# Kernel optimization log

Hardware: AMD Instinct MI355X
Metric: run time of the kernel (lower is better)

Reference implementation:

```python
import jax, jax.numpy as jnp
import numpy as np
import math

SEQ = 2048
D_MODEL = 1024
HEADS = 16
D_K = D_MODEL // HEADS
B = 2


def setup_inputs() -> dict:
    key = jax.random.key(0)
    k1, k2, k3, k4, k5 = jax.random.split(key, 5)
    s = 1.0 / math.sqrt(D_MODEL)
    x = jax.random.normal(k1, (B, SEQ, D_MODEL), dtype=jnp.float32)
    w_qkv = jax.random.normal(k2, (D_MODEL, 3 * D_MODEL), dtype=jnp.float32) * s
    b_qkv = jax.random.normal(k3, (3 * D_MODEL,), dtype=jnp.float32) * 0.01
    w_out = jax.random.normal(k4, (D_MODEL, D_MODEL), dtype=jnp.float32) * s
    b_out = jax.random.normal(k5, (D_MODEL,), dtype=jnp.float32) * 0.01
    return {"x": x, "w_qkv": w_qkv, "b_qkv": b_qkv, "w_out": w_out, "b_out": b_out}


def _rope_tables():
    inv_freq = 1.0 / (10000.0 ** (jnp.arange(0, D_K, 2, dtype=jnp.float32) / D_K))
    angles = jnp.arange(SEQ, dtype=jnp.float32)[:, None] * inv_freq[None, :]  # [S, d_k/2]
    return jnp.sin(angles), jnp.cos(angles)


def _apply_rope(x, sin, cos):
    # x: [H, B, S, d_k]; interleaved pairing: x1 = even lanes, x2 = odd lanes
    xp = x.reshape(*x.shape[:-1], D_K // 2, 2)
    x1, x2 = xp[..., 0], xp[..., 1]
    r1 = x1 * cos - x2 * sin
    r2 = x1 * sin + x2 * cos
    return jnp.stack([r1, r2], axis=-1).reshape(x.shape)


def reference(x, w_qkv, b_qkv, w_out, b_out):
    qkv = x @ w_qkv + b_qkv                     # [B, S, 3D]
    q, k, v = jnp.split(qkv, 3, axis=-1)        # each [B, S, D]

    def to_heads(t):  # chunk last dim into heads -> [H, B, S, d_k]
        return t.reshape(B, SEQ, HEADS, D_K).transpose(2, 0, 1, 3)

    q, k, v = to_heads(q), to_heads(k), to_heads(v)
    sin, cos = _rope_tables()
    q = _apply_rope(q, sin, cos)
    k = _apply_rope(k, sin, cos)

    # NOTE: original divides by scale = 1/sqrt(d_k) -> multiply by sqrt(d_k)
    scores = jnp.einsum('hbqd,hbkd->hbqk', q, k) * math.sqrt(D_K)
    causal = jnp.tril(jnp.ones((SEQ, SEQ), dtype=bool))
    scores = jnp.where(causal, scores, -jnp.inf)
    attn = jax.nn.softmax(scores, axis=-1)      # dropout_prob = 0.0
    out = jnp.einsum('hbqk,hbkd->hbqd', attn, v)  # [H, B, S, d_k]
    concat = out.transpose(1, 2, 0, 3).reshape(B, SEQ, D_MODEL)
    return concat @ w_out + b_out
```

## Files before the change

### kernel.cpp

```cpp
#include <hip/hip_runtime.h>


typedef __attribute__((ext_vector_type(8))) short s16x8;
typedef __attribute__((ext_vector_type(8))) unsigned short u16x8;
typedef __attribute__((ext_vector_type(4))) float f32x4;
typedef __attribute__((ext_vector_type(4))) int i32x4;

#define L2E 1.44269504088896340736f

__device__ __forceinline__ unsigned short f2bf(float f) {
  unsigned int u = __builtin_bit_cast(unsigned int, f);
  u += 0x7FFFu + ((u >> 16) & 1u);
  return (unsigned short)(u >> 16);
}
__device__ __forceinline__ float bf2f(unsigned short h) {
  unsigned int u = ((unsigned int)h) << 16;
  return __builtin_bit_cast(float, u);
}

__device__ __forceinline__ void gload16(const void* g, void* l) {
  __builtin_amdgcn_global_load_lds(
      (const __attribute__((address_space(1))) unsigned int*)g,
      (__attribute__((address_space(3))) unsigned int*)l, 16, 0, 0);
}

__global__ __launch_bounds__(256) void split_x_kernel(
    const float* __restrict__ x, unsigned short* __restrict__ xhi,
    unsigned short* __restrict__ xlo) {
  size_t i = ((size_t)blockIdx.x * 256 + threadIdx.x) * 8;
  f32x4 a = *(const f32x4*)(x + i);
  f32x4 c = *(const f32x4*)(x + i + 4);
  u16x8 h, lo;
#pragma unroll
  for (int j = 0; j < 4; ++j) {
    unsigned short hv = f2bf(a[j]);
    h[j] = hv; lo[j] = f2bf(a[j] - bf2f(hv));
    unsigned short hv2 = f2bf(c[j]);
    h[4 + j] = hv2; lo[4 + j] = f2bf(c[j] - bf2f(hv2));
  }
  *(u16x8*)(xhi + i) = h;
  *(u16x8*)(xlo + i) = lo;
}

__global__ __launch_bounds__(256) void transpose_split_kernel(
    const float* __restrict__ W, unsigned short* __restrict__ Thi,
    unsigned short* __restrict__ Tlo, int N, int hasLo) {
  __shared__ unsigned short hi[64][72];
  __shared__ unsigned short lo[64][72];
  const int t = threadIdx.x;
  const int k0 = blockIdx.x * 64, n0 = blockIdx.y * 64;
#pragma unroll
  for (int r = 0; r < 16; ++r) {
    int kk = r * 4 + (t >> 6);
    int nn = t & 63;
    float v = W[(size_t)(k0 + kk) * N + n0 + nn];
    unsigned short hv = f2bf(v);
    hi[nn][kk] = hv;
    lo[nn][kk] = f2bf(v - bf2f(hv));
  }
  __syncthreads();
#pragma unroll
  for (int i = 0; i < 2; ++i) {
    int ci = t + i * 256;
    int nn = ci >> 3, kc = (ci & 7) * 8;
    u16x8 vh, vl;
#pragma unroll
    for (int j = 0; j < 8; ++j) { vh[j] = hi[nn][kc + j]; vl[j] = lo[nn][kc + j]; }
    *(u16x8*)(Thi + (size_t)(n0 + nn) * 1024 + k0 + kc) = vh;
    if (hasLo) *(u16x8*)(Tlo + (size_t)(n0 + nn) * 1024 + k0 + kc) = vl;
  }
}

__global__ __launch_bounds__(256) void rope_tab_kernel(float* __restrict__ tab) {
  int idx = blockIdx.x * 256 + threadIdx.x;
  int s = idx >> 5, i = idx & 31;
  float invf = exp2f(-(float)i * 0.4152410118609203f);
  float ang = (float)s * invf;
  tab[idx] = cosf(ang);
  tab[65536 + idx] = sinf(ang);
}

__global__ __launch_bounds__(256) void gemm_qkv_kernel(
    const unsigned short* __restrict__ xhi, const unsigned short* __restrict__ xlo,
    const unsigned short* __restrict__ whi, const unsigned short* __restrict__ wlo,
    const float* __restrict__ bqkv, const float* __restrict__ ctab,
    unsigned short* __restrict__ Qsb, unsigned short* __restrict__ Ksb,
    unsigned short* __restrict__ vbufT) {
  __shared__ alignas(16) unsigned short sh[32768];
  const int tid = threadIdx.x, w = tid >> 6, l = tid & 63;
  const int l15 = l & 15, l4 = l >> 4;
  const int m0 = blockIdx.x * 128, n0 = blockIdx.y * 128;
  const int wrow = w >> 1, wcol = w & 1;
  const int which = n0 >> 10;
  const bool isV = (which == 2);
  const float* stab = ctab + 65536;
  const int g_row = l >> 2;
  const int g_col = (l & 3) * 8;

  f32x4 acc[4][4] = {};

#define STAGEP(p_) do {                                                        \
    int kk_ = (p_) * 32;                                                       \
    unsigned short* lb0_ = sh + (((p_) & 1) << 14) + (w * 2) * 512;            \
    _Pragma("unroll")                                                          \
    for (int i = 0; i < 2; ++i) {                                              \
      int rb_ = (w * 2 + i) * 16 + g_row;                                      \
      unsigned short* lb_ = lb0_ + i * 512;                                    \
      gload16(xhi + (size_t)(m0 + rb_) * 1024 + kk_ + g_col, lb_);             \
      gload16(whi + (size_t)(n0 + rb_) * 1024 + kk_ + g_col, lb_ + 4096);      \
      if (!isV) {                                                              \
        gload16(wlo + (size_t)(n0 + rb_) * 1024 + kk_ + g_col, lb_ + 8192);    \
        gload16(xlo + (size_t)(m0 + rb_) * 1024 + kk_ + g_col, lb_ + 12288);   \
      }                                                                        \
    }                                                                          \
  } while (0)

  STAGEP(0);
  __syncthreads();
  for (int p = 0; p < 32; ++p) {
    if (p + 1 < 32) STAGEP(p + 1);
    const unsigned short* bp = sh + ((p & 1) << 14);
    s16x8 af[4], bfr[4];
#pragma unroll
    for (int g = 0; g < 4; ++g) {
      af[g] = *(const s16x8*)(bp + (wrow * 64 + g * 16 + l15) * 32 + l4 * 8);
      bfr[g] = *(const s16x8*)(bp + 4096 + (wcol * 64 + g * 16 + l15) * 32 + l4 * 8);
    }
#pragma unroll
    for (int rg = 0; rg < 4; ++rg)
#pragma unroll
      for (int cg = 0; cg < 4; ++cg)
        acc[rg][cg] = __builtin_amdgcn_mfma_f32_16x16x32_bf16(af[rg], bfr[cg], acc[rg][cg], 0, 0, 0);
    if (!isV) {
      s16x8 bl[4], al[4];
#pragma unroll
      for (int g = 0; g < 4; ++g) {
        bl[g] = *(const s16x8*)(bp + 8192 + (wcol * 64 + g * 16 + l15) * 32 + l4 * 8);
        al[g] = *(const s16x8*)(bp + 12288 + (wrow * 64 + g * 16 + l15) * 32 + l4 * 8);
      }
#pragma unroll
      for (int rg = 0; rg < 4; ++rg)
#pragma unroll
        for (int cg = 0; cg < 4; ++cg)
          acc[rg][cg] = __builtin_amdgcn_mfma_f32_16x16x32_bf16(af[rg], bl[cg], acc[rg][cg], 0, 0, 0);
#pragma unroll
      for (int rg = 0; rg < 4; ++rg)
#pragma unroll
        for (int cg = 0; cg < 4; ++cg)
          acc[rg][cg] = __builtin_amdgcn_mfma_f32_16x16x32_bf16(al[rg], bfr[cg], acc[rg][cg], 0, 0, 0);
    }
    __syncthreads();
  }
#undef STAGEP

  const int n_head0 = (n0 & 1023) >> 6;
  const int bb = m0 >> 11;
  const int s_base = m0 & 2047;
  unsigned short* stg = sh;

  if (isV) {
#pragma unroll
    for (int cg = 0; cg < 4; ++cg) {
      int n_local = wcol * 64 + cg * 16 + l15;
      float bias = bqkv[n0 + n_local];
      int swz = (n_local & 7) << 3;
#pragma unroll
      for (int rg = 0; rg < 4; ++rg)
#pragma unroll
        for (int r = 0; r < 4; ++r) {
          int m_local = wrow * 64 + rg * 16 + l4 * 4 + r;
          stg[n_local * 128 + (m_local ^ swz)] = f2bf(acc[rg][cg][r] + bias);
        }
    }
    __syncthreads();
#pragma unroll
    for (int i = 0; i < 8; ++i) {
      int c = i * 256 + tid;
      int n = c >> 4, piece = c & 15;
      int hh = n_head0 + (n >> 6), d = n & 63;
      unsigned short* dst =
          vbufT + ((size_t)(bb * 16 + hh)) * 131072 + d * 2048 + s_base + piece * 8;
      *(i32x4*)dst = *(const i32x4*)(stg + n * 128 + ((piece * 8) ^ ((n & 7) << 3)));
    }
  } else {
    unsigned short* qk = which ? Ksb : Qsb;
    const float sc8 = which ? 1.0f : 8.0f;
#pragma unroll
    for (int cg = 0; cg < 4; ++cg) {
      int n_local = wcol * 64 + cg * 16 + l15;
      int dk = n_local & 63;
      int ih = dk >> 1;
      float bias = bqkv[n0 + n_local];
#pragma unroll
      for (int rg = 0; rg < 4; ++rg)
#pragma unroll
        for (int r = 0; r < 4; ++r) {
          int s = s_base + wrow * 64 + rg * 16 + l4 * 4 + r;
          float v = acc[rg][cg][r] + bias;
          float p = __shfl_xor(v, 1);
          float cs = ctab[(s << 5) + ih];
          float sn = stab[(s << 5) + ih];
          float rr = (dk & 1) ? (p * sn + v * cs) : (v * cs - p * sn);
          acc[rg][cg][r] = rr * sc8;
        }
    }
#pragma unroll
    for (int pass = 0; pass < 2; ++pass) {
#pragma unroll
      for (int cg = 0; cg < 4; ++cg) {
        int n_local = wcol * 64 + cg * 16 + l15;
#pragma unroll
        for (int rg = 0; rg < 4; ++rg)
#pragma unroll
          for (int r = 0; r < 4; ++r) {
            int m_local = wrow * 64 + rg * 16 + l4 * 4 + r;
            float rr = acc[rg][cg][r];
            unsigned short hv = f2bf(rr);
            stg[m_local * 128 + n_local] = pass ? f2bf(rr - bf2f(hv)) : hv;
          }
      }
      __syncthreads();
#pragma unroll
      for (int i = 0; i < 8; ++i) {
        int c = i * 256 + tid;
        int hh_l = c >> 10, row = (c >> 3) & 127, piece = c & 7;
        int hh = n_head0 + hh_l;
        unsigned short* dst =
            qk + (((size_t)bb * 16 + hh) * 2048 + s_base + row) * 128 + pass * 64;
        *(i32x4*)(dst + piece * 8) = *(const i32x4*)(stg + row * 128 + hh_l * 64 + piece * 8);
      }
      __syncthreads();
    }
  }
}

__global__ __launch_bounds__(512, 4) void flash_kernel(
    const unsigned short* __restrict__ Qs, const unsigned short* __restrict__ Ks,
    const unsigned short* __restrict__ VbT, unsigned short* __restrict__ attn) {
  __shared__ alignas(16) unsigned short Khi[2][64 * 64];
  __shared__ alignas(16) unsigned short Klo[2][64 * 64];
  __shared__ alignas(16) unsigned short Vt[2][64 * 64];
  __shared__ alignas(16) unsigned short Pl[8][16 * 64];

  const int tid = threadIdx.x;
  const int wv = tid >> 6, l = tid & 63;
  const int l15 = l & 15, l4 = l >> 4;

  const int sid = blockIdx.x;
  const int idx = (sid & 255) >> 5;
  const int strip = (sid >> 8) ? idx : 15 - idx;
  const int hb = sid & 31;
  const int h = hb & 15, b = hb >> 4;
  const int qb = strip * 128;

  const size_t bh = (size_t)(b * 16 + h);
  const unsigned short* Qbase = Qs + bh * 2048 * 128;
  const unsigned short* Kbase = Ks + bh * 2048 * 128;
  const unsigned short* Vbase = VbT + bh * 131072;

  s16x8 qf[2][2];
  {
    int q = qb + wv * 16 + l15;
    const unsigned short* qr = Qbase + (size_t)q * 128;
#pragma unroll
    for (int ks = 0; ks < 2; ++ks) {
      qf[0][ks] = *(const s16x8*)(qr + ks * 32 + l4 * 8);
      qf[1][ks] = *(const s16x8*)(qr + 64 + ks * 32 + l4 * 8);
    }
  }

  s16x8 vones;
#pragma unroll
  for (int j = 0; j < 8; ++j) vones[j] = (short)0x3F80;

  f32x4 acc[4] = {};
  f32x4 accl = {};
  float mrow[4];
#pragma unroll
  for (int r = 0; r < 4; ++r) mrow[r] = -1e38f;

  const int row = tid >> 3;
  const int cb = (tid & 7) * 16;

  i32x4 kh, kl, vv;
#define PREF(kt_) do {                                                        \
    int kv0_ = (kt_) * 64;                                                    \
    const char* s_ = (const char*)(Kbase + (size_t)(kv0_ + row) * 128);       \
    kh = *(const i32x4*)(s_ + cb);  kl = *(const i32x4*)(s_ + 128 + cb);      \
    vv = *(const i32x4*)((const char*)(Vbase + (size_t)row * 2048 + kv0_) + cb); \
  } while (0)

#define STAGE(bf_) do {                                                       \
    int sw = cb ^ ((row & 7) << 4);                                           \
    *(i32x4*)((char*)Khi[bf_] + row * 128 + sw) = kh;                         \
    *(i32x4*)((char*)Klo[bf_] + row * 128 + sw) = kl;                         \
    *(i32x4*)((char*)Vt[bf_] + row * 128 + sw) = vv;                          \
  } while (0)

  const int nt = (qb >> 6) + 2;
  PREF(0);
  STAGE(0);
  if (nt > 1) PREF(1);
  __syncthreads();

  for (int kt = 0; kt < nt; ++kt) {
    const int kv0 = kt * 64;
    const int cur = kt & 1;
    if (kt + 1 < nt) {
      STAGE(cur ^ 1);
      if (kt + 2 < nt) PREF(kt + 2);
    }

    f32x4 sc[4];
#pragma unroll
    for (int cg = 0; cg < 4; ++cg) {
      int kr = cg * 16 + l15;
      int swz = (kr & 7) << 4;
      const char* ph = (const char*)Khi[cur] + kr * 128;
      const char* pl2 = (const char*)Klo[cur] + kr * 128;
      s16x8 kbh[2], kbl[2];
#pragma unroll
      for (int ks = 0; ks < 2; ++ks) {
        int off = (ks * 64 + l4 * 16) ^ swz;
        kbh[ks] = *(const s16x8*)(ph + off);
        kbl[ks] = *(const s16x8*)(pl2 + off);
      }
      __builtin_amdgcn_s_setprio(1);
      f32x4 a = {0.f, 0.f, 0.f, 0.f};
#pragma unroll
      for (int ks = 0; ks < 2; ++ks) {
        a = __builtin_amdgcn_mfma_f32_16x16x32_bf16(qf[0][ks], kbh[ks], a, 0, 0, 0);
        a = __builtin_amdgcn_mfma_f32_16x16x32_bf16(qf[0][ks], kbl[ks], a, 0, 0, 0);
        a = __builtin_amdgcn_mfma_f32_16x16x32_bf16(qf[1][ks], kbh[ks], a, 0, 0, 0);
      }
      __builtin_amdgcn_s_setprio(0);
      sc[cg] = a;
    }

    if (kt >= (qb >> 6)) {
#pragma unroll
      for (int cg = 0; cg < 4; ++cg)
#pragma unroll
        for (int r = 0; r < 4; ++r) {
          int q = qb + wv * 16 + l4 * 4 + r;
          int kv = kv0 + cg * 16 + l15;
          if (kv > q) sc[cg][r] = -1e38f;
        }
    }

    {
      float vmax[4];
      bool cnd = true;
#pragma unroll
      for (int r = 0; r < 4; ++r) {
        float v = fmaxf(fmaxf(sc[0][r], sc[1][r]), fmaxf(sc[2][r], sc[3][r]));
        v = fmaxf(v, __shfl_xor(v, 1));
        v = fmaxf(v, __shfl_xor(v, 2));
        v = fmaxf(v, __shfl_xor(v, 4));
        v = fmaxf(v, __shfl_xor(v, 8));
        vmax[r] = v;
        cnd = cnd && (v <= mrow[r] + 8.0f);
      }
      const bool defer = __all(cnd ? 1 : 0);
      if (!defer) {
#pragma unroll
        for (int r = 0; r < 4; ++r) {
          float mn = fmaxf(mrow[r], vmax[r]);
          float al = exp2f((mrow[r] - mn) * L2E);
          mrow[r] = mn;
          accl[r] *= al;
#pragma unroll
          for (int dg = 0; dg < 4; ++dg) acc[dg][r] *= al;
        }
      }
#pragma unroll
      for (int cg = 0; cg < 4; ++cg)
#pragma unroll
        for (int r = 0; r < 4; ++r)
          sc[cg][r] = exp2f((sc[cg][r] - mrow[r]) * L2E);
#pragma unroll
      for (int cg = 0; cg < 4; ++cg)
#pragma unroll
        for (int r = 0; r < 4; ++r) {
          int roww = l4 * 4 + r;
          int colb = (cg * 16 + l15) * 2;
          int addr = roww * 128 + (colb ^ ((roww & 7) << 4));
          *(unsigned short*)((char*)Pl[wv] + addr) = f2bf(sc[cg][r]);
        }
    }

    {
      s16x8 pf[2];
      int swz = (l15 & 7) << 4;
#pragma unroll
      for (int kc = 0; kc < 2; ++kc)
        pf[kc] = *(const s16x8*)((const char*)Pl[wv] + l15 * 128 + ((kc * 64 + l4 * 16) ^ swz));
      __builtin_amdgcn_s_setprio(1);
#pragma unroll
      for (int dg = 0; dg < 4; ++dg) {
        int dr = dg * 16 + l15;
        int swzd = (dr & 7) << 4;
#pragma unroll
        for (int kc = 0; kc < 2; ++kc) {
          s16x8 vf = *(const s16x8*)((const char*)Vt[cur] + dr * 128 + ((kc * 64 + l4 * 16) ^ swzd));
          acc[dg] = __builtin_amdgcn_mfma_f32_16x16x32_bf16(pf[kc], vf, acc[dg], 0, 0, 0);
        }
      }
#pragma unroll
      for (int kc = 0; kc < 2; ++kc)
        accl = __builtin_amdgcn_mfma_f32_16x16x32_bf16(pf[kc], vones, accl, 0, 0, 0);
      __builtin_amdgcn_s_setprio(0);
    }
    __syncthreads();
  }
#undef PREF
#undef STAGE

  {
    unsigned short* stg = (unsigned short*)Pl;
#pragma unroll
    for (int r = 0; r < 4; ++r) {
      float inv = 1.0f / accl[r];
      int row_local = wv * 16 + l4 * 4 + r;
#pragma unroll
      for (int dg = 0; dg < 4; ++dg)
        stg[row_local * 64 + dg * 16 + l15] = f2bf(acc[dg][r] * inv);
    }
    __syncthreads();
#pragma unroll
    for (int i = 0; i < 2; ++i) {
      int c = i * 512 + tid;
      int rw = c >> 3, piece = c & 7;
      unsigned short* dst = attn + ((size_t)(b * 2048 + qb + rw)) * 1024 + h * 64;
      *(i32x4*)(dst + piece * 8) = *(const i32x4*)(stg + rw * 64 + piece * 8);
    }
  }
}

__global__ __launch_bounds__(256) void gemm_out_kernel(
    const unsigned short* __restrict__ attn, const unsigned short* __restrict__ wot,
    const float* __restrict__ bout, float* __restrict__ out) {
  __shared__ alignas(16) unsigned short sh[16384];
  const int tid = threadIdx.x, w = tid >> 6, l = tid & 63;
  const int l15 = l & 15, l4 = l >> 4;
  const int m0 = blockIdx.x * 128, n0 = blockIdx.y * 128;
  const int wrow = w >> 1, wcol = w & 1;
  const int g_row = l >> 2, g_col = (l & 3) * 8;

  f32x4 acc[4][4] = {};

#define STAGEP(p_) do {                                                        \
    int kk_ = (p_) * 32;                                                       \
    unsigned short* lb0_ = sh + (((p_) & 1) << 13) + (w * 2) * 512;            \
    _Pragma("unroll")                                                          \
    for (int i = 0; i < 2; ++i) {                                              \
      int rb_ = (w * 2 + i) * 16 + g_row;                                      \
      unsigned short* lb_ = lb0_ + i * 512;                                    \
      gload16(attn + (size_t)(m0 + rb_) * 1024 + kk_ + g_col, lb_);            \
      gload16(wot + (size_t)(n0 + rb_) * 1024 + kk_ + g_col, lb_ + 4096);      \
    }                                                                          \
  } while (0)

  STAGEP(0);
  __syncthreads();
  for (int p = 0; p < 32; ++p) {
    if (p + 1 < 32) STAGEP(p + 1);
    const unsigned short* bp = sh + ((p & 1) << 13);
    s16x8 af[4], bfr[4];
#pragma unroll
    for (int g = 0; g < 4; ++g) {
      af[g] = *(const s16x8*)(bp + (wrow * 64 + g * 16 + l15) * 32 + l4 * 8);
      bfr[g] = *(const s16x8*)(bp + 4096 + (wcol * 64 + g * 16 + l15) * 32 + l4 * 8);
    }
#pragma unroll
    for (int rg = 0; rg < 4; ++rg)
#pragma unroll
      for (int cg = 0; cg < 4; ++cg)
        acc[rg][cg] = __builtin_amdgcn_mfma_f32_16x16x32_bf16(af[rg], bfr[cg], acc[rg][cg], 0, 0, 0);
    __syncthreads();
  }
#undef STAGEP

#pragma unroll
  for (int cg = 0; cg < 4; ++cg) {
    int n = n0 + wcol * 64 + cg * 16 + l15;
    float bias = bout[n];
#pragma unroll
    for (int rg = 0; rg < 4; ++rg) {
#pragma unroll
      for (int r = 0; r < 4; ++r) {
        int m = m0 + wrow * 64 + rg * 16 + l4 * 4 + r;
        out[(size_t)m * 1024 + n] = acc[rg][cg][r] + bias;
      }
    }
  }
}

#define OFF_XHI 0ull
#define OFF_ATT 0ull
#define OFF_XLO 8388608ull
#define OFF_WHI 16777216ull
#define OFF_WLO 23068672ull
#define OFF_WOT 29360128ull
#define OFF_QS  31457280ull
#define OFF_KS  48234496ull
#define OFF_V   65011712ull

extern "C" void kernel_launch(void* const* d_in, const int* in_sizes, int n_in,
                              void* d_out, int out_size, void* d_ws, size_t ws_size,
                              hipStream_t stream) {
  (void)in_sizes; (void)n_in; (void)out_size; (void)ws_size;
  const float* x     = (const float*)d_in[0];
  const float* w_qkv = (const float*)d_in[1];
  const float* b_qkv = (const float*)d_in[2];
  const float* w_out = (const float*)d_in[3];
  const float* b_out = (const float*)d_in[4];
  float* out = (float*)d_out;
  char* ws = (char*)d_ws;

  unsigned short* xhi = (unsigned short*)(ws + OFF_XHI);
  unsigned short* xlo = (unsigned short*)(ws + OFF_XLO);
  unsigned short* whi = (unsigned short*)(ws + OFF_WHI);
  unsigned short* wlo = (unsigned short*)(ws + OFF_WLO);
  unsigned short* wot = (unsigned short*)(ws + OFF_WOT);
  unsigned short* Qsb = (unsigned short*)(ws + OFF_QS);
  unsigned short* Ksb = (unsigned short*)(ws + OFF_KS);
  unsigned short* vbT = (unsigned short*)(ws + OFF_V);
  unsigned short* att = (unsigned short*)(ws + OFF_ATT);

  float* rtab = out;

  split_x_kernel<<<2048, 256, 0, stream>>>(x, xhi, xlo);
  transpose_split_kernel<<<dim3(16, 48), 256, 0, stream>>>(w_qkv, whi, wlo, 3072, 1);
  transpose_split_kernel<<<dim3(16, 16), 256, 0, stream>>>(w_out, wot, nullptr, 1024, 0);
  rope_tab_kernel<<<256, 256, 0, stream>>>(rtab);
  gemm_qkv_kernel<<<dim3(32, 24), 256, 0, stream>>>(xhi, xlo, whi, wlo, b_qkv, rtab, Qsb, Ksb, vbT);
  flash_kernel<<<512, 512, 0, stream>>>(Qsb, Ksb, vbT, att);
  gemm_out_kernel<<<dim3(32, 8), 256, 0, stream>>>(att, wot, b_out, out);
}
```

Baseline: 192.7 us.

## Load GEMM MFMA fragments directly from global memory into registers, bypassing LDS

Both the QKV and output projection GEMMs drop the LDS double-buffered staging via global_load_lds and instead load MFMA operand fragments straight from global memory into registers. A two-deep register ping-pong overlaps the next fragment loads with the current MFMAs and removes the per-iteration __syncthreads. This gives up LDS sharing, so each wave reloads A and B tiles that other waves also read, which raises global/L2 traffic and register pressure. Each lane also makes 16-byte reads strided across rows, which may coalesce worse.

```diff
diff --git a/kernel.cpp b/kernel.cpp
--- a/kernel.cpp
+++ b/kernel.cpp
@@ -16,12 +16,6 @@
 __device__ __forceinline__ float bf2f(unsigned short h) {
   unsigned int u = ((unsigned int)h) << 16;
   return __builtin_bit_cast(float, u);
-}
-
-__device__ __forceinline__ void gload16(const void* g, void* l) {
-  __builtin_amdgcn_global_load_lds(
-      (const __attribute__((address_space(1))) unsigned int*)g,
-      (__attribute__((address_space(3))) unsigned int*)l, 16, 0, 0);
 }
 
 __global__ __launch_bounds__(256) void split_x_kernel(
@@ -86,7 +80,7 @@
     const float* __restrict__ bqkv, const float* __restrict__ ctab,
     unsigned short* __restrict__ Qsb, unsigned short* __restrict__ Ksb,
     unsigned short* __restrict__ vbufT) {
-  __shared__ alignas(16) unsigned short sh[32768];
+  __shared__ alignas(16) unsigned short sh[16384];
   const int tid = threadIdx.x, w = tid >> 6, l = tid & 63;
   const int l15 = l & 15, l4 = l >> 4;
   const int m0 = blockIdx.x * 128, n0 = blockIdx.y * 128;
@@ -94,64 +88,66 @@
   const int which = n0 >> 10;
   const bool isV = (which == 2);
   const float* stab = ctab + 65536;
-  const int g_row = l >> 2;
-  const int g_col = (l & 3) * 8;
+
+  const unsigned short* Ah = xhi + (size_t)(m0 + wrow * 64 + l15) * 1024 + l4 * 8;
+  const unsigned short* Al = xlo + (size_t)(m0 + wrow * 64 + l15) * 1024 + l4 * 8;
+  const unsigned short* Bh = whi + (size_t)(n0 + wcol * 64 + l15) * 1024 + l4 * 8;
+  const unsigned short* Bl = wlo + (size_t)(n0 + wcol * 64 + l15) * 1024 + l4 * 8;
 
   f32x4 acc[4][4] = {};
 
-#define STAGEP(p_) do {                                                        \
-    int kk_ = (p_) * 32;                                                       \
-    unsigned short* lb0_ = sh + (((p_) & 1) << 14) + (w * 2) * 512;            \
+#define LOADF(ah_, bh_, al_, bl_, p_) do {                                     \
     _Pragma("unroll")                                                          \
-    for (int i = 0; i < 2; ++i) {                                              \
-      int rb_ = (w * 2 + i) * 16 + g_row;                                      \
-      unsigned short* lb_ = lb0_ + i * 512;                                    \
-      gload16(xhi + (size_t)(m0 + rb_) * 1024 + kk_ + g_col, lb_);             \
-      gload16(whi + (size_t)(n0 + rb_) * 1024 + kk_ + g_col, lb_ + 4096);      \
-      if (!isV) {                                                              \
-        gload16(wlo + (size_t)(n0 + rb_) * 1024 + kk_ + g_col, lb_ + 8192);    \
-        gload16(xlo + (size_t)(m0 + rb_) * 1024 + kk_ + g_col, lb_ + 12288);   \
+    for (int g = 0; g < 4; ++g) {                                              \
+      ah_[g] = *(const s16x8*)(Ah + g * 16384 + (p_) * 32);                    \
+      bh_[g] = *(const s16x8*)(Bh + g * 16384 + (p_) * 32);                    \
+    }                                                                          \
+    if (!isV) {                                                                \
+      _Pragma("unroll")                                                        \
+      for (int g = 0; g < 4; ++g) {                                            \
+        al_[g] = *(const s16x8*)(Al + g * 16384 + (p_) * 32);                  \
+        bl_[g] = *(const s16x8*)(Bl + g * 16384 + (p_) * 32);                  \
       }                                                                        \
     }                                                                          \
   } while (0)
 
-  STAGEP(0);
-  __syncthreads();
-  for (int p = 0; p < 32; ++p) {
-    if (p + 1 < 32) STAGEP(p + 1);
-    const unsigned short* bp = sh + ((p & 1) << 14);
-    s16x8 af[4], bfr[4];
-#pragma unroll
-    for (int g = 0; g < 4; ++g) {
-      af[g] = *(const s16x8*)(bp + (wrow * 64 + g * 16 + l15) * 32 + l4 * 8);
-      bfr[g] = *(const s16x8*)(bp + 4096 + (wcol * 64 + g * 16 + l15) * 32 + l4 * 8);
-    }
-#pragma unroll
-    for (int rg = 0; rg < 4; ++rg)
-#pragma unroll
-      for (int cg = 0; cg < 4; ++cg)
-        acc[rg][cg] = __builtin_amdgcn_mfma_f32_16x16x32_bf16(af[rg], bfr[cg], acc[rg][cg], 0, 0, 0);
-    if (!isV) {
-      s16x8 bl[4], al[4];
-#pragma unroll
-      for (int g = 0; g < 4; ++g) {
-        bl[g] = *(const s16x8*)(bp + 8192 + (wcol * 64 + g * 16 + l15) * 32 + l4 * 8);
-        al[g] = *(const s16x8*)(bp + 12288 + (wrow * 64 + g * 16 + l15) * 32 + l4 * 8);
-      }
-#pragma unroll
-      for (int rg = 0; rg < 4; ++rg)
-#pragma unroll
-        for (int cg = 0; cg < 4; ++cg)
-          acc[rg][cg] = __builtin_amdgcn_mfma_f32_16x16x32_bf16(af[rg], bl[cg], acc[rg][cg], 0, 0, 0);
-#pragma unroll
-      for (int rg = 0; rg < 4; ++rg)
-#pragma unroll
-        for (int cg = 0; cg < 4; ++cg)
-          acc[rg][cg] = __builtin_amdgcn_mfma_f32_16x16x32_bf16(al[rg], bfr[cg], acc[rg][cg], 0, 0, 0);
-    }
-    __syncthreads();
-  }
-#undef STAGEP
+#define MFMAS(ah_, bh_, al_, bl_) do {                                         \
+    _Pragma("unroll")                                                          \
+    for (int rg = 0; rg < 4; ++rg)                                             \
+      _Pragma("unroll")                                                        \
+      for (int cg = 0; cg < 4; ++cg)                                           \
+        acc[rg][cg] = __builtin_amdgcn_mfma_f32_16x16x32_bf16(                 \
+            ah_[rg], bh_[cg], acc[rg][cg], 0, 0, 0);                           \
+    if (!isV) {                                                                \
+      _Pragma("unroll")                                                        \
+      for (int rg = 0; rg < 4; ++rg)                                           \
+        _Pragma("unroll")                                                      \
+        for (int cg = 0; cg < 4; ++cg)                                         \
+          acc[rg][cg] = __builtin_amdgcn_mfma_f32_16x16x32_bf16(               \
+              ah_[rg], bl_[cg], acc[rg][cg], 0, 0, 0);                         \
+      _Pragma("unroll")                                                        \
+      for (int rg = 0; rg < 4; ++rg)                                           \
+        _Pragma("unroll")                                                      \
+        for (int cg = 0; cg < 4; ++cg)                                         \
+          acc[rg][cg] = __builtin_amdgcn_mfma_f32_16x16x32_bf16(               \
+              al_[rg], bh_[cg], acc[rg][cg], 0, 0, 0);                         \
+    }                                                                          \
+  } while (0)
+
+  {
+    s16x8 ah0[4], bh0[4], al0[4], bl0[4];
+    s16x8 ah1[4], bh1[4], al1[4], bl1[4];
+    LOADF(ah0, bh0, al0, bl0, 0);
+#pragma unroll 1
+    for (int pp = 0; pp < 16; ++pp) {
+      LOADF(ah1, bh1, al1, bl1, 2 * pp + 1);
+      MFMAS(ah0, bh0, al0, bl0);
+      if (pp < 15) LOADF(ah0, bh0, al0, bl0, 2 * pp + 2);
+      MFMAS(ah1, bh1, al1, bl1);
+    }
+  }
+#undef LOADF
+#undef MFMAS
 
   const int n_head0 = (n0 & 1023) >> 6;
   const int bb = m0 >> 11;
@@ -440,46 +436,46 @@
 __global__ __launch_bounds__(256) void gemm_out_kernel(
     const unsigned short* __restrict__ attn, const unsigned short* __restrict__ wot,
     const float* __restrict__ bout, float* __restrict__ out) {
-  __shared__ alignas(16) unsigned short sh[16384];
   const int tid = threadIdx.x, w = tid >> 6, l = tid & 63;
   const int l15 = l & 15, l4 = l >> 4;
   const int m0 = blockIdx.x * 128, n0 = blockIdx.y * 128;
   const int wrow = w >> 1, wcol = w & 1;
-  const int g_row = l >> 2, g_col = (l & 3) * 8;
+
+  const unsigned short* Ab = attn + (size_t)(m0 + wrow * 64 + l15) * 1024 + l4 * 8;
+  const unsigned short* Bb = wot + (size_t)(n0 + wcol * 64 + l15) * 1024 + l4 * 8;
 
   f32x4 acc[4][4] = {};
 
-#define STAGEP(p_) do {                                                        \
-    int kk_ = (p_) * 32;                                                       \
-    unsigned short* lb0_ = sh + (((p_) & 1) << 13) + (w * 2) * 512;            \
+#define LOADF(a_, b_, p_) do {                                                 \
     _Pragma("unroll")                                                          \
-    for (int i = 0; i < 2; ++i) {                                              \
-      int rb_ = (w * 2 + i) * 16 + g_row;                                      \
-      unsigned short* lb_ = lb0_ + i * 512;                                    \
-      gload16(attn + (size_t)(m0 + rb_) * 1024 + kk_ + g_col, lb_);            \
-      gload16(wot + (size_t)(n0 + rb_) * 1024 + kk_ + g_col, lb_ + 4096);      \
+    for (int g = 0; g < 4; ++g) {                                              \
+      a_[g] = *(const s16x8*)(Ab + g * 16384 + (p_) * 32);                     \
+      b_[g] = *(const s16x8*)(Bb + g * 16384 + (p_) * 32);                     \
     }                                                                          \
   } while (0)
 
-  STAGEP(0);
-  __syncthreads();
-  for (int p = 0; p < 32; ++p) {
-    if (p + 1 < 32) STAGEP(p + 1);
-    const unsigned short* bp = sh + ((p & 1) << 13);
-    s16x8 af[4], bfr[4];
-#pragma unroll
-    for (int g = 0; g < 4; ++g) {
-      af[g] = *(const s16x8*)(bp + (wrow * 64 + g * 16 + l15) * 32 + l4 * 8);
-      bfr[g] = *(const s16x8*)(bp + 4096 + (wcol * 64 + g * 16 + l15) * 32 + l4 * 8);
-    }
-#pragma unroll
-    for (int rg = 0; rg < 4; ++rg)
-#pragma unroll
-      for (int cg = 0; cg < 4; ++cg)
-        acc[rg][cg] = __builtin_amdgcn_mfma_f32_16x16x32_bf16(af[rg], bfr[cg], acc[rg][cg], 0, 0, 0);
-    __syncthreads();
-  }
-#undef STAGEP
+#define MFMAS(a_, b_) do {                                                     \
+    _Pragma("unroll")                                                          \
+    for (int rg = 0; rg < 4; ++rg)                                             \
+      _Pragma("unroll")                                                        \
+      for (int cg = 0; cg < 4; ++cg)                                           \
+        acc[rg][cg] = __builtin_amdgcn_mfma_f32_16x16x32_bf16(                 \
+            a_[rg], b_[cg], acc[rg][cg], 0, 0, 0);                             \
+  } while (0)
+
+  {
+    s16x8 a0[4], b0[4], a1[4], b1[4];
+    LOADF(a0, b0, 0);
+#pragma unroll 1
+    for (int pp = 0; pp < 16; ++pp) {
+      LOADF(a1, b1, 2 * pp + 1);
+      MFMAS(a0, b0);
+      if (pp < 15) LOADF(a0, b0, 2 * pp + 2);
+      MFMAS(a1, b1);
+    }
+  }
+#undef LOADF
+#undef MFMAS
 
 #pragma unroll
   for (int cg = 0; cg < 4; ++cg) {
```

New measurement: 286.1 us. +48.5%, slower.
